# Kernel tuning notes

Measured on AMD Instinct MI355X. Metric: run time of the kernel, lower is better.

## Reference

```python
import jax, jax.numpy as jnp
import numpy as np

N_HEADS = 16
D_MODEL = 1024
D_HEAD = D_MODEL // N_HEADS


def setup_inputs() -> dict:
    key = jax.random.key(0)
    ks = jax.random.split(key, 5)
    scale = 0.02
    x = jax.random.normal(ks[0], (2, 2048, D_MODEL), dtype=jnp.float32)
    # torch.nn.Linear weights: (out_features, in_features)
    w_in = jax.random.normal(ks[1], (3 * D_MODEL, D_MODEL), dtype=jnp.float32) * scale
    b_in = jax.random.normal(ks[2], (3 * D_MODEL,), dtype=jnp.float32) * scale
    w_out = jax.random.normal(ks[3], (D_MODEL, D_MODEL), dtype=jnp.float32) * scale
    b_out = jax.random.normal(ks[4], (D_MODEL,), dtype=jnp.float32) * scale
    return {"x": x, "w_in": w_in, "b_in": b_in, "w_out": w_out, "b_out": b_out}


def reference(x, w_in, b_in, w_out, b_out):
    B, S, D = x.shape
    H, Dh = N_HEADS, D_HEAD
    qkv = x @ w_in.T + b_in                      # [B,S,3D]
    q, k, v = jnp.split(qkv, 3, axis=-1)
    q = q.reshape(B, S, H, Dh).transpose(0, 2, 1, 3)  # [B,H,S,Dh]
    k = k.reshape(B, S, H, Dh).transpose(0, 2, 1, 3)
    v = v.reshape(B, S, H, Dh).transpose(0, 2, 1, 3)
    scores = jnp.einsum('bhqd,bhkd->bhqk', q, k) / jnp.sqrt(jnp.float32(Dh))
    weights = jax.nn.softmax(scores, axis=-1)
    out = jnp.einsum('bhqk,bhkd->bhqd', weights, v)   # [B,H,S,Dh]
    # Faithful to original: reshape WITHOUT transposing heads back
    out = out.reshape(B, S, D)
    return out @ w_out.T + b_out
```

## Files before the change

kernel.cpp:

```cpp
#include <hip/hip_runtime.h>
#include <math.h>

constexpr int D_MODEL = 1024;
constexpr int N_HEADS = 16;
constexpr int D_HEAD  = 64;
constexpr int SEQ     = 2048;
constexpr int BATCH   = 2;
constexpr int M_ROWS  = BATCH * SEQ;
constexpr int QKV_N   = 3 * D_MODEL;
constexpr int KDIM    = 1024;
constexpr int NROWS   = BATCH * N_HEADS * SEQ;

typedef __bf16 bf16x8 __attribute__((ext_vector_type(8)));
typedef float  f32x4  __attribute__((ext_vector_type(4)));
typedef float  f32x16 __attribute__((ext_vector_type(16)));
typedef unsigned uint2v __attribute__((ext_vector_type(2)));

union U4 { uint4 u; bf16x8 b; ushort s[8]; };

__device__ __forceinline__ unsigned pk2bf(float lo, float hi) {
    union { unsigned u; __bf16 b[2]; } cv;
    cv.b[0] = (__bf16)lo; cv.b[1] = (__bf16)hi;
    return cv.u;
}
__device__ __forceinline__ ushort f2bf(float f) {
    union { ushort s[2]; __bf16 b[2]; } cv;
    cv.b[0] = (__bf16)f;
    return cv.s[0];
}

__device__ __forceinline__ int swz(int row, int bytecol) {
    return row * 128 + (bytecol ^ ((row & 7) << 4));
}

__device__ __forceinline__ void gload16(const void* g, void* l) {
    __builtin_amdgcn_global_load_lds(
        (const __attribute__((address_space(1))) unsigned int*)g,
        (__attribute__((address_space(3))) unsigned int*)l, 16, 0, 0);
}

#define QSCALE 0.18033688011112042f

__device__ __forceinline__ void pack_paf(const f32x16& s, bf16x8& f0o, bf16x8& f1o) {
    const unsigned q0 = pk2bf(s[0],  s[1]);
    const unsigned q1 = pk2bf(s[2],  s[3]);
    const unsigned q2 = pk2bf(s[4],  s[5]);
    const unsigned q3 = pk2bf(s[6],  s[7]);
    const unsigned q4 = pk2bf(s[8],  s[9]);
    const unsigned q5 = pk2bf(s[10], s[11]);
    const unsigned q6 = pk2bf(s[12], s[13]);
    const unsigned q7 = pk2bf(s[14], s[15]);
    const uint2v x = __builtin_amdgcn_permlane32_swap(q0, q2, false, false);
    const uint2v y = __builtin_amdgcn_permlane32_swap(q1, q3, false, false);
    const uint2v z = __builtin_amdgcn_permlane32_swap(q4, q6, false, false);
    const uint2v u = __builtin_amdgcn_permlane32_swap(q5, q7, false, false);
    U4 f0; f0.u.x = x[0]; f0.u.y = y[0]; f0.u.z = x[1]; f0.u.w = y[1];
    U4 f1; f1.u.x = z[0]; f1.u.y = u[0]; f1.u.z = z[1]; f1.u.w = u[1];
    f0o = f0.b; f1o = f1.b;
}

__global__ __launch_bounds__(256)
void convert3_kernel(const float* __restrict__ x,  ushort* __restrict__ xo,
                     const float* __restrict__ wi, ushort* __restrict__ wio,
                     const float* __restrict__ wo, ushort* __restrict__ woo) {
    const int na = M_ROWS * D_MODEL;
    const int nb = QKV_N * D_MODEL;
    const int nc = D_MODEL * D_MODEL;
    const int total = (na + nb + nc) / 8;
    for (int g = blockIdx.x * blockDim.x + threadIdx.x; g < total;
         g += gridDim.x * blockDim.x) {
        const int i = g * 8;
        const float* src; ushort* dst; int off;
        if (i < na)           { src = x;  dst = xo;  off = i; }
        else if (i < na + nb) { src = wi; dst = wio; off = i - na; }
        else                  { src = wo; dst = woo; off = i - na - nb; }
        const float4 a = *reinterpret_cast<const float4*>(src + off);
        const float4 b = *reinterpret_cast<const float4*>(src + off + 4);
        uint4 o;
        o.x = pk2bf(a.x, a.y); o.y = pk2bf(a.z, a.w);
        o.z = pk2bf(b.x, b.y); o.w = pk2bf(b.z, b.w);
        *reinterpret_cast<uint4*>(dst + off) = o;
    }
}

__device__ __forceinline__ void mfma_gemm_bt_128(
    const ushort* __restrict__ Ag, const ushort* __restrict__ Bg,
    int m0, int n0, ushort* As, ushort* Bs, f32x4 (&acc)[4][4])
{
    const int tid = threadIdx.x;
    const int l   = tid & 63;
    const int rl  = l & 15, hh = l >> 4;
    const int w   = tid >> 6;
    const int wm  = (w >> 1) * 64, wn = (w & 1) * 64;

    const int r0 = tid >> 2;
    const int ce = (tid & 3) * 8;
    const ushort* gA0 = Ag + (size_t)(m0 + r0) * KDIM + ce;
    const ushort* gA1 = gA0 + (size_t)64 * KDIM;
    const ushort* gB0 = Bg + (size_t)(n0 + r0) * KDIM + ce;
    const ushort* gB1 = gB0 + (size_t)64 * KDIM;
    char* lA = (char*)As + tid * 16;
    char* lB = (char*)Bs + tid * 16;

    for (int k0 = 0; k0 < KDIM; k0 += 32) {
        __syncthreads();
        gload16(gA0 + k0, lA);
        gload16(gA1 + k0, lA + 4096);
        gload16(gB0 + k0, lB);
        gload16(gB1 + k0, lB + 4096);
        __syncthreads();

        bf16x8 af[4], bf_[4];
        #pragma unroll
        for (int f = 0; f < 4; ++f)
            af[f]  = *(const bf16x8*)((const char*)As + (wm + f * 16 + rl) * 64 + hh * 16);
        #pragma unroll
        for (int f = 0; f < 4; ++f)
            bf_[f] = *(const bf16x8*)((const char*)Bs + (wn + f * 16 + rl) * 64 + hh * 16);
        #pragma unroll
        for (int i = 0; i < 4; ++i)
            #pragma unroll
            for (int j = 0; j < 4; ++j)
                acc[i][j] = __builtin_amdgcn_mfma_f32_16x16x32_bf16(af[i], bf_[j], acc[i][j], 0, 0, 0);
    }
}

__global__ __launch_bounds__(256)
void qkv_mfma_kernel(const ushort* __restrict__ xb, const ushort* __restrict__ wb,
                     const float* __restrict__ b_in,
                     ushort* __restrict__ Q, ushort* __restrict__ K, ushort* __restrict__ V) {
    __shared__ __align__(16) ushort As[128 * 32];
    __shared__ __align__(16) ushort Bs[128 * 32];

    f32x4 acc[4][4];
    #pragma unroll
    for (int i = 0; i < 4; ++i)
        #pragma unroll
        for (int j = 0; j < 4; ++j) acc[i][j] = (f32x4){0.f, 0.f, 0.f, 0.f};

    const int m0 = blockIdx.y * 128, n0 = blockIdx.x * 128;
    mfma_gemm_bt_128(xb, wb, m0, n0, As, Bs, acc);

    const int l  = threadIdx.x & 63, w = threadIdx.x >> 6;
    const int rl = l & 15, hh = l >> 4;
    const int mb = m0 + (w >> 1) * 64, nb = n0 + (w & 1) * 64;

    #pragma unroll
    for (int j = 0; j < 4; ++j) {
        const int n  = nb + j * 16 + rl;
        const float bias = b_in[n];
        const int t  = n >> 10;
        const int jj = n & 1023;
        const int h  = jj >> 6;
        const int d  = jj & 63;
        ushort* dst = (t == 0) ? Q : (t == 1) ? K : V;
        const float sc = (t == 0) ? QSCALE : 1.0f;
        #pragma unroll
        for (int i = 0; i < 4; ++i)
            #pragma unroll
            for (int r = 0; r < 4; ++r) {
                const int m = mb + i * 16 + hh * 4 + r;
                const int b = m >> 11;
                const int s = m & (SEQ - 1);
                dst[((size_t)(b * N_HEADS + h) * SEQ + s) * D_HEAD + d] =
                    f2bf((acc[i][j][r] + bias) * sc);
            }
    }
}

__global__ __launch_bounds__(256)
void attn_mfma_split_kernel(const ushort* __restrict__ Q, const ushort* __restrict__ K,
                            const ushort* __restrict__ V, ushort* __restrict__ Op,
                            float* __restrict__ lbuf) {
    __shared__ __align__(16) char Ks[2][64 * 128];
    __shared__ __align__(16) char Vs[2][64 * 128];

    const int tid = threadIdx.x;
    const int w   = tid >> 6;
    const int l   = tid & 63;
    const int l31 = l & 31;
    const int lh  = l >> 5;

    const int bid  = blockIdx.x;
    const int nid  = (bid & 7) * 64 + (bid >> 3);
    const int bh   = nid >> 4;
    const int rem  = nid & 15;
    const int half = rem >> 3;
    const int qt   = rem & 7;

    const size_t base  = (size_t)bh * SEQ * D_HEAD;
    const size_t kbase = base + (size_t)half * 1024 * D_HEAD;
    const int qbase = qt * 256 + w * 64;

    bf16x8 qfA[4], qfB[4];
    {
        const ushort* qpA = Q + base + (size_t)(qbase + l31) * D_HEAD + lh * 8;
        const ushort* qpB = qpA + (size_t)32 * D_HEAD;
        #pragma unroll
        for (int c = 0; c < 4; ++c) {
            U4 ta; ta.u = *(const uint4*)(qpA + c * 16); qfA[c] = ta.b;
            U4 tb; tb.u = *(const uint4*)(qpB + c * 16); qfB[c] = tb.b;
        }
    }

    f32x16 otA0, otA1, otB0, otB1;
    #pragma unroll
    for (int r = 0; r < 16; ++r) { otA0[r] = 0.f; otA1[r] = 0.f; otB0[r] = 0.f; otB1[r] = 0.f; }
    float lA = 0.0f, lB = 0.0f;

    const int sr  = tid >> 2, seg = tid & 3;
    const int kp  = (tid & 31) * 2, db = tid >> 5;
    const ushort* gK  = K + kbase + (size_t)sr * D_HEAD + seg * 8;
    const ushort* gV0 = V + kbase + (size_t)kp * D_HEAD + db * 8;
    const ushort* gV1 = gV0 + D_HEAD;

    uint4 ka, kb; U4 va, vb;
    ka   = *(const uint4*)(gK);
    kb   = *(const uint4*)(gK + 32);
    va.u = *(const uint4*)(gV0);
    vb.u = *(const uint4*)(gV1);
    {
        char* kd = Ks[0]; char* vd = Vs[0];
        *(uint4*)(kd + swz(sr, seg * 16))      = ka;
        *(uint4*)(kd + swz(sr, seg * 16 + 64)) = kb;
        #pragma unroll
        for (int i = 0; i < 8; ++i) {
            const int d = db * 8 + i;
            *(unsigned*)(vd + d * 128 + ((kp * 2) ^ ((d & 7) << 4))) =
                (unsigned)va.s[i] | ((unsigned)vb.s[i] << 16);
        }
    }

    constexpr int NT = 1024 / 64;
    for (int t = 0; t < NT; ++t) {
        const int cur = t & 1;
        __syncthreads();

        if (t + 1 < NT) {
            const size_t off = (size_t)(t + 1) * 64 * D_HEAD;
            ka   = *(const uint4*)(gK + off);
            kb   = *(const uint4*)(gK + off + 32);
            va.u = *(const uint4*)(gV0 + off);
            vb.u = *(const uint4*)(gV1 + off);
        }
        const char* kbuf = Ks[cur];
        const char* vbuf = Vs[cur];

        f32x16 sA0, sA1, sB0, sB1;
        #pragma unroll
        for (int r = 0; r < 16; ++r) { sA0[r] = 0.f; sA1[r] = 0.f; sB0[r] = 0.f; sB1[r] = 0.f; }
        #pragma unroll
        for (int c = 0; c < 4; ++c) {
            const bf16x8 kf0 = *(const bf16x8*)(kbuf + swz(l31, c * 32 + lh * 16));
            sA0 = __builtin_amdgcn_mfma_f32_32x32x16_bf16(kf0, qfA[c], sA0, 0, 0, 0);
            sB0 = __builtin_amdgcn_mfma_f32_32x32x16_bf16(kf0, qfB[c], sB0, 0, 0, 0);
            const bf16x8 kf1 = *(const bf16x8*)(kbuf + swz(32 + l31, c * 32 + lh * 16));
            sA1 = __builtin_amdgcn_mfma_f32_32x32x16_bf16(kf1, qfA[c], sA1, 0, 0, 0);
            sB1 = __builtin_amdgcn_mfma_f32_32x32x16_bf16(kf1, qfB[c], sB1, 0, 0, 0);
        }

        float psA = 0.f, psB = 0.f;
        #pragma unroll
        for (int r = 0; r < 16; ++r) {
            sA0[r] = __builtin_amdgcn_exp2f(sA0[r]); psA += sA0[r];
            sA1[r] = __builtin_amdgcn_exp2f(sA1[r]); psA += sA1[r];
            sB0[r] = __builtin_amdgcn_exp2f(sB0[r]); psB += sB0[r];
            sB1[r] = __builtin_amdgcn_exp2f(sB1[r]); psB += sB1[r];
        }
        lA += psA; lB += psB;

        bf16x8 pafA[4], pafB[4];
        pack_paf(sA0, pafA[0], pafA[1]);
        pack_paf(sA1, pafA[2], pafA[3]);
        pack_paf(sB0, pafB[0], pafB[1]);
        pack_paf(sB1, pafB[2], pafB[3]);

        #pragma unroll
        for (int kc = 0; kc < 4; ++kc) {
            const bf16x8 vf0 = *(const bf16x8*)(vbuf + swz(l31, kc * 32 + lh * 16));
            otA0 = __builtin_amdgcn_mfma_f32_32x32x16_bf16(vf0, pafA[kc], otA0, 0, 0, 0);
            otB0 = __builtin_amdgcn_mfma_f32_32x32x16_bf16(vf0, pafB[kc], otB0, 0, 0, 0);
            const bf16x8 vf1 = *(const bf16x8*)(vbuf + swz(32 + l31, kc * 32 + lh * 16));
            otA1 = __builtin_amdgcn_mfma_f32_32x32x16_bf16(vf1, pafA[kc], otA1, 0, 0, 0);
            otB1 = __builtin_amdgcn_mfma_f32_32x32x16_bf16(vf1, pafB[kc], otB1, 0, 0, 0);
        }

        if (t + 1 < NT) {
            char* kd = Ks[cur ^ 1]; char* vd = Vs[cur ^ 1];
            *(uint4*)(kd + swz(sr, seg * 16))      = ka;
            *(uint4*)(kd + swz(sr, seg * 16 + 64)) = kb;
            #pragma unroll
            for (int i = 0; i < 8; ++i) {
                const int d = db * 8 + i;
                *(unsigned*)(vd + d * 128 + ((kp * 2) ^ ((d & 7) << 4))) =
                    (unsigned)va.s[i] | ((unsigned)vb.s[i] << 16);
            }
        }
    }

    lA += __shfl_xor(lA, 32, 64);
    lB += __shfl_xor(lB, 32, 64);
    const size_t growA = (size_t)bh * SEQ + qbase + l31;
    const size_t growB = growA + 32;
    ushort* opA = Op + ((size_t)half * NROWS + growA) * D_HEAD;
    ushort* opB = Op + ((size_t)half * NROWS + growB) * D_HEAD;
    #pragma unroll
    for (int dt = 0; dt < 2; ++dt) {
        const f32x16& oa = dt ? otA1 : otA0;
        const f32x16& ob = dt ? otB1 : otB0;
        #pragma unroll
        for (int g = 0; g < 4; ++g) {
            const int d0 = dt * 32 + g * 8 + lh * 4;
            uint2 s2;
            s2.x = pk2bf(oa[g * 4 + 0], oa[g * 4 + 1]);
            s2.y = pk2bf(oa[g * 4 + 2], oa[g * 4 + 3]);
            *(uint2*)(opA + d0) = s2;
            uint2 s3;
            s3.x = pk2bf(ob[g * 4 + 0], ob[g * 4 + 1]);
            s3.y = pk2bf(ob[g * 4 + 2], ob[g * 4 + 3]);
            *(uint2*)(opB + d0) = s3;
        }
    }
    if (lh == 0) {
        lbuf[(size_t)half * NROWS + growA] = lA;
        lbuf[(size_t)half * NROWS + growB] = lB;
    }
}

__global__ __launch_bounds__(256)
void combine_kernel(const ushort* __restrict__ Op, const float* __restrict__ lbuf,
                    ushort* __restrict__ A) {
    const int idx = blockIdx.x * 256 + threadIdx.x;
    const int row = idx >> 3;
    const int dc  = (idx & 7) * 8;
    const float inv = 1.0f / (lbuf[row] + lbuf[NROWS + row]);
    U4 o1, o2;
    o1.u = *(const uint4*)(Op + (size_t)row * D_HEAD + dc);
    o2.u = *(const uint4*)(Op + ((size_t)NROWS + row) * D_HEAD + dc);
    uint4 r;
    float v[8];
    #pragma unroll
    for (int i = 0; i < 8; ++i)
        v[i] = ((float)o1.b[i] + (float)o2.b[i]) * inv;
    r.x = pk2bf(v[0], v[1]); r.y = pk2bf(v[2], v[3]);
    r.z = pk2bf(v[4], v[5]); r.w = pk2bf(v[6], v[7]);
    *(uint4*)(A + (size_t)row * D_HEAD + dc) = r;
}

__global__ __launch_bounds__(256)
void out_mfma_kernel(const ushort* __restrict__ Ab, const ushort* __restrict__ wb,
                     const float* __restrict__ b_out, float* __restrict__ out) {
    __shared__ __align__(16) ushort As[128 * 32];
    __shared__ __align__(16) ushort Bs[128 * 32];

    f32x4 acc[4][4];
    #pragma unroll
    for (int i = 0; i < 4; ++i)
        #pragma unroll
        for (int j = 0; j < 4; ++j) acc[i][j] = (f32x4){0.f, 0.f, 0.f, 0.f};

    const int m0 = blockIdx.y * 128, n0 = blockIdx.x * 128;
    mfma_gemm_bt_128(Ab, wb, m0, n0, As, Bs, acc);

    const int l  = threadIdx.x & 63, w = threadIdx.x >> 6;
    const int rl = l & 15, hh = l >> 4;
    const int mb = m0 + (w >> 1) * 64, nb = n0 + (w & 1) * 64;

    #pragma unroll
    for (int j = 0; j < 4; ++j) {
        const int n = nb + j * 16 + rl;
        const float bias = b_out[n];
        #pragma unroll
        for (int i = 0; i < 4; ++i)
            #pragma unroll
            for (int r = 0; r < 4; ++r) {
                const int m = mb + i * 16 + hh * 4 + r;
                out[(size_t)m * D_MODEL + n] = acc[i][j][r] + bias;
            }
    }
}

extern "C" void kernel_launch(void* const* d_in, const int* in_sizes, int n_in,
                              void* d_out, int out_size, void* d_ws, size_t ws_size,
                              hipStream_t stream) {
    const float* x     = (const float*)d_in[0];
    const float* w_in  = (const float*)d_in[1];
    const float* b_in  = (const float*)d_in[2];
    const float* w_out = (const float*)d_in[3];
    const float* b_out = (const float*)d_in[4];
    float* out = (float*)d_out;

    const size_t T = (size_t)BATCH * N_HEADS * SEQ * D_HEAD;
    ushort* Qw  = (ushort*)d_ws;
    ushort* Kw  = Qw + T;
    ushort* Vw  = Kw + T;
    ushort* Opw = Vw + T;
    ushort* xb  = Opw + T;
    ushort* wib = xb + T;
    ushort* wob = wib + (size_t)QKV_N * D_MODEL;
    float*  lw  = (float*)(wob + (size_t)D_MODEL * D_MODEL);
    ushort* Aw  = Qw;

    convert3_kernel<<<2048, 256, 0, stream>>>(x, xb, w_in, wib, w_out, wob);

    qkv_mfma_kernel<<<dim3(QKV_N / 128, M_ROWS / 128), 256, 0, stream>>>(
        xb, wib, b_in, Qw, Kw, Vw);
    attn_mfma_split_kernel<<<512, 256, 0, stream>>>(Qw, Kw, Vw, Opw, lw);
    combine_kernel<<<NROWS * 8 / 256, 256, 0, stream>>>(Opw, lw, Aw);
    out_mfma_kernel<<<dim3(D_MODEL / 128, M_ROWS / 128), 256, 0, stream>>>(
        Aw, wob, b_out, out);
}
```

Measured before the change: 136.6 us.

## Load K tiles direct to LDS and split S-tile processing to cut registers

K tiles are now fetched with direct global-to-LDS loads (gload16) into a pre-swizzled layout instead of passing through registers. The QK^T/softmax/PV step is split into two 32-key halves so only two score accumulators are live at once. Launch bounds now request 3 blocks per CU. Together these aim to lower VGPR pressure and raise occupancy, at the cost of less MFMA batching per half and reliance on the gload16 helper and its swizzle matching swz().

```diff
diff --git a/kernel.cpp b/kernel.cpp
--- a/kernel.cpp
+++ b/kernel.cpp
@@ -168,7 +168,7 @@
     }
 }
 
-__global__ __launch_bounds__(256)
+__global__ __launch_bounds__(256, 3)
 void attn_mfma_split_kernel(const ushort* __restrict__ Q, const ushort* __restrict__ K,
                             const ushort* __restrict__ V, ushort* __restrict__ Op,
                             float* __restrict__ lbuf) {
@@ -208,21 +208,21 @@
     for (int r = 0; r < 16; ++r) { otA0[r] = 0.f; otA1[r] = 0.f; otB0[r] = 0.f; otB1[r] = 0.f; }
     float lA = 0.0f, lB = 0.0f;
 
-    const int sr  = tid >> 2, seg = tid & 3;
-    const int kp  = (tid & 31) * 2, db = tid >> 5;
-    const ushort* gK  = K + kbase + (size_t)sr * D_HEAD + seg * 8;
+    const int krow = tid >> 3, kch = tid & 7;
+    const int kcg  = kch ^ (krow & 7);
+    const ushort* gK = K + kbase + (size_t)krow * D_HEAD + kcg * 8;
+
+    const int kp = (tid & 31) * 2, db = tid >> 5;
     const ushort* gV0 = V + kbase + (size_t)kp * D_HEAD + db * 8;
     const ushort* gV1 = gV0 + D_HEAD;
 
-    uint4 ka, kb; U4 va, vb;
-    ka   = *(const uint4*)(gK);
-    kb   = *(const uint4*)(gK + 32);
+    gload16(gK, Ks[0] + tid * 16);
+    gload16(gK + 2048, Ks[0] + tid * 16 + 4096);
+    U4 va, vb;
     va.u = *(const uint4*)(gV0);
     vb.u = *(const uint4*)(gV1);
     {
-        char* kd = Ks[0]; char* vd = Vs[0];
-        *(uint4*)(kd + swz(sr, seg * 16))      = ka;
-        *(uint4*)(kd + swz(sr, seg * 16 + 64)) = kb;
+        char* vd = Vs[0];
         #pragma unroll
         for (int i = 0; i < 8; ++i) {
             const int d = db * 8 + i;
@@ -238,57 +238,56 @@
 
         if (t + 1 < NT) {
             const size_t off = (size_t)(t + 1) * 64 * D_HEAD;
-            ka   = *(const uint4*)(gK + off);
-            kb   = *(const uint4*)(gK + off + 32);
+            gload16(gK + off,        Ks[cur ^ 1] + tid * 16);
+            gload16(gK + off + 2048, Ks[cur ^ 1] + tid * 16 + 4096);
             va.u = *(const uint4*)(gV0 + off);
             vb.u = *(const uint4*)(gV1 + off);
         }
         const char* kbuf = Ks[cur];
         const char* vbuf = Vs[cur];
 
-        f32x16 sA0, sA1, sB0, sB1;
-        #pragma unroll
-        for (int r = 0; r < 16; ++r) { sA0[r] = 0.f; sA1[r] = 0.f; sB0[r] = 0.f; sB1[r] = 0.f; }
-        #pragma unroll
-        for (int c = 0; c < 4; ++c) {
-            const bf16x8 kf0 = *(const bf16x8*)(kbuf + swz(l31, c * 32 + lh * 16));
-            sA0 = __builtin_amdgcn_mfma_f32_32x32x16_bf16(kf0, qfA[c], sA0, 0, 0, 0);
-            sB0 = __builtin_amdgcn_mfma_f32_32x32x16_bf16(kf0, qfB[c], sB0, 0, 0, 0);
-            const bf16x8 kf1 = *(const bf16x8*)(kbuf + swz(32 + l31, c * 32 + lh * 16));
-            sA1 = __builtin_amdgcn_mfma_f32_32x32x16_bf16(kf1, qfA[c], sA1, 0, 0, 0);
-            sB1 = __builtin_amdgcn_mfma_f32_32x32x16_bf16(kf1, qfB[c], sB1, 0, 0, 0);
-        }
-
-        float psA = 0.f, psB = 0.f;
-        #pragma unroll
-        for (int r = 0; r < 16; ++r) {
-            sA0[r] = __builtin_amdgcn_exp2f(sA0[r]); psA += sA0[r];
-            sA1[r] = __builtin_amdgcn_exp2f(sA1[r]); psA += sA1[r];
-            sB0[r] = __builtin_amdgcn_exp2f(sB0[r]); psB += sB0[r];
-            sB1[r] = __builtin_amdgcn_exp2f(sB1[r]); psB += sB1[r];
-        }
-        lA += psA; lB += psB;
-
-        bf16x8 pafA[4], pafB[4];
-        pack_paf(sA0, pafA[0], pafA[1]);
-        pack_paf(sA1, pafA[2], pafA[3]);
-        pack_paf(sB0, pafB[0], pafB[1]);
-        pack_paf(sB1, pafB[2], pafB[3]);
-
-        #pragma unroll
-        for (int kc = 0; kc < 4; ++kc) {
-            const bf16x8 vf0 = *(const bf16x8*)(vbuf + swz(l31, kc * 32 + lh * 16));
-            otA0 = __builtin_amdgcn_mfma_f32_32x32x16_bf16(vf0, pafA[kc], otA0, 0, 0, 0);
-            otB0 = __builtin_amdgcn_mfma_f32_32x32x16_bf16(vf0, pafB[kc], otB0, 0, 0, 0);
-            const bf16x8 vf1 = *(const bf16x8*)(vbuf + swz(32 + l31, kc * 32 + lh * 16));
-            otA1 = __builtin_amdgcn_mfma_f32_32x32x16_bf16(vf1, pafA[kc], otA1, 0, 0, 0);
-            otB1 = __builtin_amdgcn_mfma_f32_32x32x16_bf16(vf1, pafB[kc], otB1, 0, 0, 0);
+        #pragma unroll
+        for (int s = 0; s < 2; ++s) {
+            f32x16 stA, stB;
+            #pragma unroll
+            for (int r = 0; r < 16; ++r) { stA[r] = 0.f; stB[r] = 0.f; }
+            #pragma unroll
+            for (int c = 0; c < 4; ++c) {
+                const bf16x8 kf = *(const bf16x8*)(kbuf + swz(s * 32 + l31, c * 32 + lh * 16));
+                stA = __builtin_amdgcn_mfma_f32_32x32x16_bf16(kf, qfA[c], stA, 0, 0, 0);
+                stB = __builtin_amdgcn_mfma_f32_32x32x16_bf16(kf, qfB[c], stB, 0, 0, 0);
+            }
+
+            float a0 = 0.f, a1 = 0.f, b0 = 0.f, b1 = 0.f;
+            #pragma unroll
+            for (int r = 0; r < 8; ++r) {
+                stA[r]     = __builtin_amdgcn_exp2f(stA[r]);     a0 += stA[r];
+                stA[8 + r] = __builtin_amdgcn_exp2f(stA[8 + r]); a1 += stA[8 + r];
+                stB[r]     = __builtin_amdgcn_exp2f(stB[r]);     b0 += stB[r];
+                stB[8 + r] = __builtin_amdgcn_exp2f(stB[8 + r]); b1 += stB[8 + r];
+            }
+            lA += a0 + a1; lB += b0 + b1;
+
+            bf16x8 pA0, pA1, pB0, pB1;
+            pack_paf(stA, pA0, pA1);
+            pack_paf(stB, pB0, pB1);
+
+            #pragma unroll
+            for (int k2 = 0; k2 < 2; ++k2) {
+                const int kc = s * 2 + k2;
+                const bf16x8 vf0 = *(const bf16x8*)(vbuf + swz(l31,      kc * 32 + lh * 16));
+                const bf16x8 vf1 = *(const bf16x8*)(vbuf + swz(32 + l31, kc * 32 + lh * 16));
+                const bf16x8 pA = k2 ? pA1 : pA0;
+                const bf16x8 pB = k2 ? pB1 : pB0;
+                otA0 = __builtin_amdgcn_mfma_f32_32x32x16_bf16(vf0, pA, otA0, 0, 0, 0);
+                otB0 = __builtin_amdgcn_mfma_f32_32x32x16_bf16(vf0, pB, otB0, 0, 0, 0);
+                otA1 = __builtin_amdgcn_mfma_f32_32x32x16_bf16(vf1, pA, otA1, 0, 0, 0);
+                otB1 = __builtin_amdgcn_mfma_f32_32x32x16_bf16(vf1, pB, otB1, 0, 0, 0);
+            }
         }
 
         if (t + 1 < NT) {
-            char* kd = Ks[cur ^ 1]; char* vd = Vs[cur ^ 1];
-            *(uint4*)(kd + swz(sr, seg * 16))      = ka;
-            *(uint4*)(kd + swz(sr, seg * 16 + 64)) = kb;
+            char* vd = Vs[cur ^ 1];
             #pragma unroll
             for (int i = 0; i < 8; ++i) {
                 const int d = db * 8 + i;
```

After: 157.9 us. +15.6%, slower.
